# Kernel tuning notes

Hardware: AMD Instinct MI355X
Metric: run time of the kernel (lower is better)

The kernel has to match this reference:

```python
import jax, jax.numpy as jnp
import numpy as np

N_NODES = 50000
N_EDGES = 800000
IN_FEATS = 128
HID_FEATS = 128
NUM_CLASSES = 32


def setup_inputs() -> dict:
    key = jax.random.key(0)
    ks = jax.random.split(key, 7)
    node_embeddings = jax.random.normal(ks[0], (N_NODES, IN_FEATS), jnp.float32)
    edge_encodings = jax.random.normal(ks[1], (N_EDGES, 16), jnp.float32)
    W1 = jax.random.normal(ks[2], (IN_FEATS, HID_FEATS), jnp.float32) / jnp.sqrt(jnp.float32(IN_FEATS))
    b1 = jnp.zeros((HID_FEATS,), jnp.float32)
    W2 = jax.random.normal(ks[3], (HID_FEATS, NUM_CLASSES), jnp.float32) / jnp.sqrt(jnp.float32(HID_FEATS))
    b2 = jnp.zeros((NUM_CLASSES,), jnp.float32)
    edge_index = jax.random.randint(ks[4], (2, N_EDGES), 0, N_NODES, jnp.int32)
    return {"node_embeddings": node_embeddings, "edge_encodings": edge_encodings,
            "W1": W1, "b1": b1, "W2": W2, "b2": b2, "edge_index": edge_index}


def _graph_conv(x, W, b, src, dst, d_out, d_in, n_nodes):
    # DGL GraphConv, norm='both': out = D_in^{-1/2} A D_out^{-1/2} x W + b
    # Apply weight first (out_feats <= in_feats) -- associativity, same math.
    h = (x @ W) * d_out[:, None]            # [N, F_out], source-side norm
    agg = jax.ops.segment_sum(h[src], dst, num_segments=n_nodes)  # SpMM
    return agg * d_in[:, None] + b


def reference(node_embeddings, edge_encodings, W1, b1, W2, b2, edge_index):
    src, dst = edge_index[0], edge_index[1]
    n = node_embeddings.shape[0]
    ones = jnp.ones(src.shape, jnp.float32)
    out_deg = jax.ops.segment_sum(ones, src, num_segments=n)
    in_deg = jax.ops.segment_sum(ones, dst, num_segments=n)
    d_out = jnp.where(out_deg > 0, out_deg, 1.0) ** -0.5
    d_in = jnp.where(in_deg > 0, in_deg, 1.0) ** -0.5
    h = jax.nn.relu(_graph_conv(node_embeddings, W1, b1, src, dst, d_out, d_in, n))
    return _graph_conv(h, W2, b2, src, dst, d_out, d_in, n)
```

## Files before the change

### kernel.cpp

```cpp
#include <hip/hip_runtime.h>


#define F 128
#define C 32
#define PADN 50176
#define SCAN_BLOCKS 49
#define HB 256
#define PADN4 (PADN / 4)

using bf16x8 = __attribute__((ext_vector_type(8))) short;
using f32x4  = __attribute__((ext_vector_type(4))) float;

static __device__ __forceinline__ unsigned short bf16_bits(float f) {
    union { float f; unsigned int u; } v; v.f = f;
    unsigned int r = v.u + 0x7fffu + ((v.u >> 16) & 1u);
    return (unsigned short)(r >> 16);
}

__global__ void passA_kernel(const int* __restrict__ dst, int* __restrict__ cnt_in,
                             unsigned short* __restrict__ pos, int E) {
    int e = blockIdx.x * blockDim.x + threadIdx.x;
    if (e >= E) return;
    int p = atomicAdd(&cnt_in[dst[e]], 1);
    pos[e] = (unsigned short)p;
}

__global__ __launch_bounds__(256) void hist_out_kernel(
    const int* __restrict__ src, unsigned int* __restrict__ partial, int E) {
    __shared__ unsigned int h[PADN4];
    const int tid = threadIdx.x;
    for (int j = tid; j < PADN4; j += 256) h[j] = 0u;
    __syncthreads();
    const int per = (E + HB - 1) / HB;
    const int lo = blockIdx.x * per;
    const int hi = min(E, lo + per);
    for (int e = lo + tid; e < hi; e += 256) {
        int v = src[e];
        atomicAdd(&h[v >> 2], 1u << ((v & 3) * 8));
    }
    __syncthreads();
    unsigned int* p = partial + (size_t)blockIdx.x * PADN4;
    for (int j = tid; j < PADN4; j += 256) p[j] = h[j];
}

__global__ void reduce_dinv_kernel(const unsigned int* __restrict__ partial,
                                   const int* __restrict__ cnt_in,
                                   float* __restrict__ dinv_out, float* __restrict__ dinv_in,
                                   int n4) {
    int i = blockIdx.x * blockDim.x + threadIdx.x;
    if (i >= n4) return;
    unsigned int s0 = 0, s1 = 0, s2 = 0, s3 = 0;
#pragma unroll 8
    for (int b = 0; b < HB; ++b) {
        unsigned int w = partial[(size_t)b * PADN4 + i];
        s0 += w & 0xffu; s1 += (w >> 8) & 0xffu; s2 += (w >> 16) & 0xffu; s3 += w >> 24;
    }
    int base = i * 4;
    dinv_out[base + 0] = s0 ? rsqrtf((float)s0) : 1.0f;
    dinv_out[base + 1] = s1 ? rsqrtf((float)s1) : 1.0f;
    dinv_out[base + 2] = s2 ? rsqrtf((float)s2) : 1.0f;
    dinv_out[base + 3] = s3 ? rsqrtf((float)s3) : 1.0f;
    int4 c = *(const int4*)(cnt_in + base);
    dinv_in[base + 0] = c.x > 0 ? rsqrtf((float)c.x) : 1.0f;
    dinv_in[base + 1] = c.y > 0 ? rsqrtf((float)c.y) : 1.0f;
    dinv_in[base + 2] = c.z > 0 ? rsqrtf((float)c.z) : 1.0f;
    dinv_in[base + 3] = c.w > 0 ? rsqrtf((float)c.w) : 1.0f;
}

__global__ __launch_bounds__(256) void scan1_kernel(const int* __restrict__ cnt,
                                                    int* __restrict__ part, int* __restrict__ bsum) {
    __shared__ int sdata[256];
    const int tid = threadIdx.x;
    const int base = blockIdx.x * 1024 + tid * 4;
    int4 c = *(const int4*)(cnt + base);
    int s = c.x + c.y + c.z + c.w;
    sdata[tid] = s;
    __syncthreads();
    for (int off = 1; off < 256; off <<= 1) {
        int v = 0;
        if (tid >= off) v = sdata[tid - off];
        __syncthreads();
        if (tid >= off) sdata[tid] += v;
        __syncthreads();
    }
    int excl = sdata[tid] - s;
    part[base]     = excl;
    part[base + 1] = excl + c.x;
    part[base + 2] = excl + c.x + c.y;
    part[base + 3] = excl + c.x + c.y + c.z;
    if (tid == 255) bsum[blockIdx.x] = sdata[255];
}

__global__ __launch_bounds__(256) void scan2_kernel(int* __restrict__ bsum, int nb) {
    __shared__ int sdata[256];
    const int tid = threadIdx.x;
    int v = (tid < nb) ? bsum[tid] : 0;
    sdata[tid] = v;
    __syncthreads();
    for (int off = 1; off < 256; off <<= 1) {
        int t = 0;
        if (tid >= off) t = sdata[tid - off];
        __syncthreads();
        if (tid >= off) sdata[tid] += t;
        __syncthreads();
    }
    if (tid < nb) bsum[tid] = sdata[tid] - v;
}

__global__ void scan3_kernel(int* __restrict__ row_ptr, const int* __restrict__ bsum, int n) {
    int i = blockIdx.x * blockDim.x + threadIdx.x;
    if (i >= n) return;
    row_ptr[i] += bsum[i >> 10];
}

__global__ void fillB_kernel(const int* __restrict__ src, const int* __restrict__ dst,
                             const unsigned short* __restrict__ pos,
                             const int* __restrict__ row_ptr, int* __restrict__ eidx, int E) {
    int e = blockIdx.x * blockDim.x + threadIdx.x;
    if (e >= E) return;
    eidx[row_ptr[dst[e]] + pos[e]] = src[e];
}

__global__ __launch_bounds__(256) void gemm1_mfma_kernel(
    const float* __restrict__ X, const float* __restrict__ W,
    const float* __restrict__ dinv_out, unsigned short* __restrict__ H1, int N) {
    __shared__ unsigned short w1t[128 * 136];
    const int tid = threadIdx.x;
#pragma unroll
    for (int p = 0; p < 16; ++p) {
        int k = p * 8 + (tid >> 5);
        int c4 = (tid & 31) * 4;
        float4 v = *(const float4*)(W + k * 128 + c4);
        w1t[(c4 + 0) * 136 + k] = bf16_bits(v.x);
        w1t[(c4 + 1) * 136 + k] = bf16_bits(v.y);
        w1t[(c4 + 2) * 136 + k] = bf16_bits(v.z);
        w1t[(c4 + 3) * 136 + k] = bf16_bits(v.w);
    }
    __syncthreads();

    const int lane = tid & 63;
    const int wave = tid >> 6;
    const int row0 = blockIdx.x * 64 + wave * 16;
    const int arow = row0 + (lane & 15);
    const int asrc = (arow < N) ? arow : 0;
    const int kg = (lane >> 4) * 8;

    f32x4 acc[8];
#pragma unroll
    for (int n = 0; n < 8; ++n) acc[n] = (f32x4){0.f, 0.f, 0.f, 0.f};

#pragma unroll
    for (int kk = 0; kk < 4; ++kk) {
        const float* xp = X + (size_t)asrc * F + kk * 32 + kg;
        float4 xa = *(const float4*)(xp);
        float4 xb = *(const float4*)(xp + 4);
        bf16x8 a;
        a[0] = (short)bf16_bits(xa.x); a[1] = (short)bf16_bits(xa.y);
        a[2] = (short)bf16_bits(xa.z); a[3] = (short)bf16_bits(xa.w);
        a[4] = (short)bf16_bits(xb.x); a[5] = (short)bf16_bits(xb.y);
        a[6] = (short)bf16_bits(xb.z); a[7] = (short)bf16_bits(xb.w);
#pragma unroll
        for (int n = 0; n < 8; ++n) {
            const bf16x8 b = *(const bf16x8*)(w1t + (n * 16 + (lane & 15)) * 136 + kk * 32 + kg);
            acc[n] = __builtin_amdgcn_mfma_f32_16x16x32_bf16(a, b, acc[n], 0, 0, 0);
        }
    }

    const int rbase = row0 + (lane >> 4) * 4;
#pragma unroll
    for (int j = 0; j < 4; ++j) {
        int r = rbase + j;
        if (r < N) {
            float s = dinv_out[r];
            unsigned short* out = H1 + (size_t)r * F + (lane & 15);
#pragma unroll
            for (int n = 0; n < 8; ++n) out[n * 16] = bf16_bits(acc[n][j] * s);
        }
    }
}

__global__ __launch_bounds__(256) void spmm_csr1_kernel(
    const unsigned short* __restrict__ H1, const int* __restrict__ row_ptr,
    const int* __restrict__ cnt, const int* __restrict__ eidx,
    float* __restrict__ AGG1, int N) {
    int node = blockIdx.x * 4 + (threadIdx.x >> 6);
    if (node >= N) return;
    const int l = threadIdx.x & 63;
    const int start = row_ptr[node];
    const int deg = cnt[node];
    const unsigned int* Hb = (const unsigned int*)H1 + l;
    float2 a0 = {0.f,0.f}, a1 = {0.f,0.f}, a2 = {0.f,0.f}, a3 = {0.f,0.f};
    int i = 0;
    for (; i + 3 < deg; i += 4) {
        int s0 = eidx[start + i];
        int s1 = eidx[start + i + 1];
        int s2 = eidx[start + i + 2];
        int s3 = eidx[start + i + 3];
        unsigned int w0 = Hb[(size_t)s0 * 64];
        unsigned int w1 = Hb[(size_t)s1 * 64];
        unsigned int w2 = Hb[(size_t)s2 * 64];
        unsigned int w3 = Hb[(size_t)s3 * 64];
        a0.x += __uint_as_float(w0 << 16); a0.y += __uint_as_float(w0 & 0xffff0000u);
        a1.x += __uint_as_float(w1 << 16); a1.y += __uint_as_float(w1 & 0xffff0000u);
        a2.x += __uint_as_float(w2 << 16); a2.y += __uint_as_float(w2 & 0xffff0000u);
        a3.x += __uint_as_float(w3 << 16); a3.y += __uint_as_float(w3 & 0xffff0000u);
    }
    for (; i < deg; ++i) {
        int s0 = eidx[start + i];
        unsigned int w0 = Hb[(size_t)s0 * 64];
        a0.x += __uint_as_float(w0 << 16); a0.y += __uint_as_float(w0 & 0xffff0000u);
    }
    float2 o = {a0.x + a1.x + a2.x + a3.x, a0.y + a1.y + a2.y + a3.y};
    *(float2*)(AGG1 + (size_t)node * F + l * 2) = o;
}

__global__ __launch_bounds__(256) void gemm2_kernel(
    const float* __restrict__ AGG1, const float* __restrict__ b1,
    const float* __restrict__ dinv_in, const float* __restrict__ W2,
    const float* __restrict__ dinv_out, float* __restrict__ H2, int N) {
    __shared__ float ws[F * C];
    __shared__ float xs[64 * 132];
    const int tid = threadIdx.x;
    const int rbase = blockIdx.x * 64;
    {
        float4* ws4 = (float4*)ws;
        const float4* W4 = (const float4*)W2;
#pragma unroll
        for (int j = 0; j < 4; ++j) ws4[tid + j * 256] = W4[tid + j * 256];
    }
#pragma unroll
    for (int j = 0; j < 8; ++j) {
        int i4 = tid + j * 256;
        int r = i4 >> 5, k4 = i4 & 31;
        int row = rbase + r;
        float4 v = make_float4(0.f, 0.f, 0.f, 0.f);
        float di = 0.f;
        if (row < N) {
            v = *(const float4*)(AGG1 + (size_t)row * F + k4 * 4);
            di = dinv_in[row];
        }
        float4 bb = *(const float4*)(b1 + k4 * 4);
        int base = r * 132 + k4 * 4;
        xs[base]     = fmaxf(fmaf(v.x, di, bb.x), 0.f);
        xs[base + 1] = fmaxf(fmaf(v.y, di, bb.y), 0.f);
        xs[base + 2] = fmaxf(fmaf(v.z, di, bb.z), 0.f);
        xs[base + 3] = fmaxf(fmaf(v.w, di, bb.w), 0.f);
    }
    __syncthreads();
    const int m0 = tid & 7;
    const int rr = tid >> 3;
    float4 a0 = {0,0,0,0}, a1 = {0,0,0,0};
#pragma unroll 8
    for (int k = 0; k < F; ++k) {
        float4 w = *(const float4*)(ws + k * C + m0 * 4);
        float xa = xs[(rr * 2) * 132 + k];
        float xb = xs[(rr * 2 + 1) * 132 + k];
        a0.x += xa * w.x; a0.y += xa * w.y; a0.z += xa * w.z; a0.w += xa * w.w;
        a1.x += xb * w.x; a1.y += xb * w.y; a1.z += xb * w.z; a1.w += xb * w.w;
    }
    int row0 = rbase + rr * 2;
    int row1 = row0 + 1;
    if (row0 < N) {
        float s = dinv_out[row0];
        float4 o = {a0.x * s, a0.y * s, a0.z * s, a0.w * s};
        *(float4*)(H2 + (size_t)row0 * C + m0 * 4) = o;
    }
    if (row1 < N) {
        float s = dinv_out[row1];
        float4 o = {a1.x * s, a1.y * s, a1.z * s, a1.w * s};
        *(float4*)(H2 + (size_t)row1 * C + m0 * 4) = o;
    }
}

__global__ __launch_bounds__(256) void spmm_csr2_kernel(
    const float* __restrict__ H2, const int* __restrict__ row_ptr,
    const int* __restrict__ cnt, const int* __restrict__ eidx,
    const float* __restrict__ dinv_in, const float* __restrict__ b2,
    float* __restrict__ out, int N) {
    int node = blockIdx.x * 8 + (threadIdx.x >> 5);
    if (node >= N) return;
    const int col = threadIdx.x & 31;
    const int start = row_ptr[node];
    const int deg = cnt[node];
    float acc0 = 0.f, acc1 = 0.f;
    int i = 0;
    for (; i + 1 < deg; i += 2) {
        int s0 = eidx[start + i];
        int s1 = eidx[start + i + 1];
        acc0 += H2[(size_t)s0 * C + col];
        acc1 += H2[(size_t)s1 * C + col];
    }
    if (i < deg) acc0 += H2[(size_t)eidx[start + i] * C + col];
    out[(size_t)node * C + col] = fmaf(acc0 + acc1, dinv_in[node], b2[col]);
}

extern "C" void kernel_launch(void* const* d_in, const int* in_sizes, int n_in,
                              void* d_out, int out_size, void* d_ws, size_t ws_size,
                              hipStream_t stream) {
    const float* X  = (const float*)d_in[0];
    const float* W1 = (const float*)d_in[2];
    const float* b1 = (const float*)d_in[3];
    const float* W2 = (const float*)d_in[4];
    const float* b2 = (const float*)d_in[5];
    const int*   ei = (const int*)d_in[6];

    const int N = in_sizes[0] / F;
    const int E = in_sizes[6] / 2;
    const int* src = ei;
    const int* dst = ei + E;

    float* wsf      = (float*)d_ws;
    float* dinv_out = wsf;
    float* dinv_in  = wsf + PADN;
    int* cnt_in  = (int*)(wsf + 2 * PADN);
    int* row_ptr = cnt_in + PADN;
    int* bsum    = row_ptr + PADN;
    unsigned short* pos = (unsigned short*)(bsum + 256);
    int* eidx    = (int*)(pos + E);
    unsigned short* H1 = (unsigned short*)(eidx + E);
    float* AGG1  = (float*)(H1 + (size_t)N * F);
    unsigned int* partial = (unsigned int*)AGG1;
    float* H2    = (float*)H1;
    float* outp  = (float*)d_out;

    hipMemsetAsync(cnt_in, 0, (size_t)PADN * sizeof(int), stream);

    passA_kernel<<<(E + 255) / 256, 256, 0, stream>>>(dst, cnt_in, pos, E);
    hist_out_kernel<<<HB, 256, 0, stream>>>(src, partial, E);
    reduce_dinv_kernel<<<(PADN4 + 255) / 256, 256, 0, stream>>>(partial, cnt_in, dinv_out, dinv_in, PADN4);
    scan1_kernel<<<SCAN_BLOCKS, 256, 0, stream>>>(cnt_in, row_ptr, bsum);
    scan2_kernel<<<1, 256, 0, stream>>>(bsum, SCAN_BLOCKS);
    scan3_kernel<<<PADN / 256, 256, 0, stream>>>(row_ptr, bsum, PADN);
    fillB_kernel<<<(E + 255) / 256, 256, 0, stream>>>(src, dst, pos, row_ptr, eidx, E);

    gemm1_mfma_kernel<<<(N + 63) / 64, 256, 0, stream>>>(X, W1, dinv_out, H1, N);
    spmm_csr1_kernel<<<(N + 3) / 4, 256, 0, stream>>>(H1, row_ptr, cnt_in, eidx, AGG1, N);
    gemm2_kernel<<<(N + 63) / 64, 256, 0, stream>>>(AGG1, b1, dinv_in, W2, dinv_out, H2, N);
    spmm_csr2_kernel<<<(N + 7) / 8, 256, 0, stream>>>(H2, row_ptr, cnt_in, eidx, dinv_in, b2, outp, N);
}
```

Measured before the change: 279.4 us.

## Fuse degree counting and scan kernels, store layer-2 features as bf16

Merges the in-degree atomic pass into the out-degree histogram kernel, and merges the degree reduction with the first scan stage, which removes two launches and one pass over the edge list. The layer-2 projected features are now stored as bf16 and gathered as packed pairs, with 16 lanes per node, to halve the gather traffic in the second SpMM. Trade-offs: the fused histogram kernel runs the global atomics from only 256 blocks, which may serialize them more than the old wide launch did, and bf16 storage adds rounding error to the output.

```diff
diff --git a/kernel.cpp b/kernel.cpp
--- a/kernel.cpp
+++ b/kernel.cpp
@@ -17,16 +17,10 @@
     return (unsigned short)(r >> 16);
 }
 
-__global__ void passA_kernel(const int* __restrict__ dst, int* __restrict__ cnt_in,
-                             unsigned short* __restrict__ pos, int E) {
-    int e = blockIdx.x * blockDim.x + threadIdx.x;
-    if (e >= E) return;
-    int p = atomicAdd(&cnt_in[dst[e]], 1);
-    pos[e] = (unsigned short)p;
-}
-
-__global__ __launch_bounds__(256) void hist_out_kernel(
-    const int* __restrict__ src, unsigned int* __restrict__ partial, int E) {
+__global__ __launch_bounds__(256) void passAB_kernel(
+    const int* __restrict__ src, const int* __restrict__ dst,
+    int* __restrict__ cnt_in, unsigned short* __restrict__ pos,
+    unsigned int* __restrict__ partial, int E) {
     __shared__ unsigned int h[PADN4];
     const int tid = threadIdx.x;
     for (int j = tid; j < PADN4; j += 256) h[j] = 0u;
@@ -35,6 +29,9 @@
     const int lo = blockIdx.x * per;
     const int hi = min(E, lo + per);
     for (int e = lo + tid; e < hi; e += 256) {
+        int d = dst[e];
+        int p = atomicAdd(&cnt_in[d], 1);
+        pos[e] = (unsigned short)p;
         int v = src[e];
         atomicAdd(&h[v >> 2], 1u << ((v & 3) * 8));
     }
@@ -43,19 +40,20 @@
     for (int j = tid; j < PADN4; j += 256) p[j] = h[j];
 }
 
-__global__ void reduce_dinv_kernel(const unsigned int* __restrict__ partial,
-                                   const int* __restrict__ cnt_in,
-                                   float* __restrict__ dinv_out, float* __restrict__ dinv_in,
-                                   int n4) {
-    int i = blockIdx.x * blockDim.x + threadIdx.x;
-    if (i >= n4) return;
+__global__ __launch_bounds__(256) void reduce_scan_kernel(
+    const unsigned int* __restrict__ partial, const int* __restrict__ cnt_in,
+    float* __restrict__ dinv_out, float* __restrict__ dinv_in,
+    int* __restrict__ part, int* __restrict__ bsum) {
+    __shared__ int sdata[256];
+    const int tid = threadIdx.x;
+    const int i = blockIdx.x * 256 + tid;
     unsigned int s0 = 0, s1 = 0, s2 = 0, s3 = 0;
 #pragma unroll 8
     for (int b = 0; b < HB; ++b) {
         unsigned int w = partial[(size_t)b * PADN4 + i];
         s0 += w & 0xffu; s1 += (w >> 8) & 0xffu; s2 += (w >> 16) & 0xffu; s3 += w >> 24;
     }
-    int base = i * 4;
+    const int base = i * 4;
     dinv_out[base + 0] = s0 ? rsqrtf((float)s0) : 1.0f;
     dinv_out[base + 1] = s1 ? rsqrtf((float)s1) : 1.0f;
     dinv_out[base + 2] = s2 ? rsqrtf((float)s2) : 1.0f;
@@ -65,16 +63,8 @@
     dinv_in[base + 1] = c.y > 0 ? rsqrtf((float)c.y) : 1.0f;
     dinv_in[base + 2] = c.z > 0 ? rsqrtf((float)c.z) : 1.0f;
     dinv_in[base + 3] = c.w > 0 ? rsqrtf((float)c.w) : 1.0f;
-}
-
-__global__ __launch_bounds__(256) void scan1_kernel(const int* __restrict__ cnt,
-                                                    int* __restrict__ part, int* __restrict__ bsum) {
-    __shared__ int sdata[256];
-    const int tid = threadIdx.x;
-    const int base = blockIdx.x * 1024 + tid * 4;
-    int4 c = *(const int4*)(cnt + base);
-    int s = c.x + c.y + c.z + c.w;
-    sdata[tid] = s;
+    int ssum = c.x + c.y + c.z + c.w;
+    sdata[tid] = ssum;
     __syncthreads();
     for (int off = 1; off < 256; off <<= 1) {
         int v = 0;
@@ -83,7 +73,7 @@
         if (tid >= off) sdata[tid] += v;
         __syncthreads();
     }
-    int excl = sdata[tid] - s;
+    int excl = sdata[tid] - ssum;
     part[base]     = excl;
     part[base + 1] = excl + c.x;
     part[base + 2] = excl + c.x + c.y;
@@ -217,7 +207,7 @@
 __global__ __launch_bounds__(256) void gemm2_kernel(
     const float* __restrict__ AGG1, const float* __restrict__ b1,
     const float* __restrict__ dinv_in, const float* __restrict__ W2,
-    const float* __restrict__ dinv_out, float* __restrict__ H2, int N) {
+    const float* __restrict__ dinv_out, unsigned short* __restrict__ H2, int N) {
     __shared__ float ws[F * C];
     __shared__ float xs[64 * 132];
     const int tid = threadIdx.x;
@@ -262,36 +252,47 @@
     int row1 = row0 + 1;
     if (row0 < N) {
         float s = dinv_out[row0];
-        float4 o = {a0.x * s, a0.y * s, a0.z * s, a0.w * s};
-        *(float4*)(H2 + (size_t)row0 * C + m0 * 4) = o;
+        ushort4 o;
+        o.x = bf16_bits(a0.x * s); o.y = bf16_bits(a0.y * s);
+        o.z = bf16_bits(a0.z * s); o.w = bf16_bits(a0.w * s);
+        *(ushort4*)(H2 + (size_t)row0 * C + m0 * 4) = o;
     }
     if (row1 < N) {
         float s = dinv_out[row1];
-        float4 o = {a1.x * s, a1.y * s, a1.z * s, a1.w * s};
-        *(float4*)(H2 + (size_t)row1 * C + m0 * 4) = o;
+        ushort4 o;
+        o.x = bf16_bits(a1.x * s); o.y = bf16_bits(a1.y * s);
+        o.z = bf16_bits(a1.z * s); o.w = bf16_bits(a1.w * s);
+        *(ushort4*)(H2 + (size_t)row1 * C + m0 * 4) = o;
     }
 }
 
 __global__ __launch_bounds__(256) void spmm_csr2_kernel(
-    const float* __restrict__ H2, const int* __restrict__ row_ptr,
+    const unsigned int* __restrict__ H2, const int* __restrict__ row_ptr,
     const int* __restrict__ cnt, const int* __restrict__ eidx,
     const float* __restrict__ dinv_in, const float* __restrict__ b2,
     float* __restrict__ out, int N) {
-    int node = blockIdx.x * 8 + (threadIdx.x >> 5);
+    int node = blockIdx.x * 16 + (threadIdx.x >> 4);
     if (node >= N) return;
-    const int col = threadIdx.x & 31;
+    const int l = threadIdx.x & 15;
     const int start = row_ptr[node];
     const int deg = cnt[node];
-    float acc0 = 0.f, acc1 = 0.f;
+    const unsigned int* Hb = H2 + l;
+    float2 a0 = {0.f, 0.f}, a1 = {0.f, 0.f};
     int i = 0;
     for (; i + 1 < deg; i += 2) {
-        int s0 = eidx[start + i];
-        int s1 = eidx[start + i + 1];
-        acc0 += H2[(size_t)s0 * C + col];
-        acc1 += H2[(size_t)s1 * C + col];
-    }
-    if (i < deg) acc0 += H2[(size_t)eidx[start + i] * C + col];
-    out[(size_t)node * C + col] = fmaf(acc0 + acc1, dinv_in[node], b2[col]);
+        unsigned int w0 = Hb[(size_t)eidx[start + i] * 16];
+        unsigned int w1 = Hb[(size_t)eidx[start + i + 1] * 16];
+        a0.x += __uint_as_float(w0 << 16); a0.y += __uint_as_float(w0 & 0xffff0000u);
+        a1.x += __uint_as_float(w1 << 16); a1.y += __uint_as_float(w1 & 0xffff0000u);
+    }
+    if (i < deg) {
+        unsigned int w0 = Hb[(size_t)eidx[start + i] * 16];
+        a0.x += __uint_as_float(w0 << 16); a0.y += __uint_as_float(w0 & 0xffff0000u);
+    }
+    float di = dinv_in[node];
+    float2 bb = *(const float2*)(b2 + l * 2);
+    float2 o = { fmaf(a0.x + a1.x, di, bb.x), fmaf(a0.y + a1.y, di, bb.y) };
+    *(float2*)(out + (size_t)node * C + l * 2) = o;
 }
 
 extern "C" void kernel_launch(void* const* d_in, const int* in_sizes, int n_in,
@@ -320,15 +321,13 @@
     unsigned short* H1 = (unsigned short*)(eidx + E);
     float* AGG1  = (float*)(H1 + (size_t)N * F);
     unsigned int* partial = (unsigned int*)AGG1;
-    float* H2    = (float*)H1;
+    unsigned short* H2 = H1;
     float* outp  = (float*)d_out;
 
     hipMemsetAsync(cnt_in, 0, (size_t)PADN * sizeof(int), stream);
 
-    passA_kernel<<<(E + 255) / 256, 256, 0, stream>>>(dst, cnt_in, pos, E);
-    hist_out_kernel<<<HB, 256, 0, stream>>>(src, partial, E);
-    reduce_dinv_kernel<<<(PADN4 + 255) / 256, 256, 0, stream>>>(partial, cnt_in, dinv_out, dinv_in, PADN4);
-    scan1_kernel<<<SCAN_BLOCKS, 256, 0, stream>>>(cnt_in, row_ptr, bsum);
+    passAB_kernel<<<HB, 256, 0, stream>>>(src, dst, cnt_in, pos, partial, E);
+    reduce_scan_kernel<<<SCAN_BLOCKS, 256, 0, stream>>>(partial, cnt_in, dinv_out, dinv_in, row_ptr, bsum);
     scan2_kernel<<<1, 256, 0, stream>>>(bsum, SCAN_BLOCKS);
     scan3_kernel<<<PADN / 256, 256, 0, stream>>>(row_ptr, bsum, PADN);
     fillB_kernel<<<(E + 255) / 256, 256, 0, stream>>>(src, dst, pos, row_ptr, eidx, E);
@@ -336,5 +335,5 @@
     gemm1_mfma_kernel<<<(N + 63) / 64, 256, 0, stream>>>(X, W1, dinv_out, H1, N);
     spmm_csr1_kernel<<<(N + 3) / 4, 256, 0, stream>>>(H1, row_ptr, cnt_in, eidx, AGG1, N);
     gemm2_kernel<<<(N + 63) / 64, 256, 0, stream>>>(AGG1, b1, dinv_in, W2, dinv_out, H2, N);
-    spmm_csr2_kernel<<<(N + 7) / 8, 256, 0, stream>>>(H2, row_ptr, cnt_in, eidx, dinv_in, b2, outp, N);
-}
+    spmm_csr2_kernel<<<(N + 15) / 16, 256, 0, stream>>>((const unsigned int*)H2, row_ptr, cnt_in, eidx, dinv_in, b2, outp, N);
+}
```

New measurement: 263.3 us. 1.06x faster.
